# Kernel tuning notes

Hardware: AMD Instinct MI355X
Metric: run time of the kernel (lower is better)

## Reference

```python
import jax, jax.numpy as jnp
import numpy as np

N_NODES = 200000
N_EDGES = 3200000


def _gcn_prep(edge_index, n_nodes):
    # Add self loops (PyG GCNConv default) and compute symmetric normalization.
    loops = jnp.arange(n_nodes, dtype=edge_index.dtype)
    src = jnp.concatenate([edge_index[0], loops])
    dst = jnp.concatenate([edge_index[1], loops])
    deg = jax.ops.segment_sum(jnp.ones_like(dst, dtype=jnp.float32), dst,
                              num_segments=n_nodes)
    dinv = jnp.where(deg > 0, jax.lax.rsqrt(deg), 0.0)
    norm = dinv[src] * dinv[dst]  # [E+N]
    return src, dst, norm


def _gcn_conv(x, src, dst, norm, W, b, n_nodes):
    h = x @ W                                   # [N, out]
    msg = h[src] * norm[:, None]                # gather + scale, [E+N, out]
    out = jax.ops.segment_sum(msg, dst, num_segments=n_nodes)  # scatter-add
    return out + b


def setup_inputs() -> dict:
    key = jax.random.key(0)
    k = jax.random.split(key, 4)
    x = jax.random.normal(k[0], (N_NODES, 4), dtype=jnp.float32)
    edge_index = jax.random.randint(k[1], (2, N_EDGES), 0, N_NODES, dtype=jnp.int64)
    W1 = jax.random.normal(k[2], (4, 16), dtype=jnp.float32) * (1.0 / np.sqrt(4))
    b1 = jnp.zeros((16,), dtype=jnp.float32)
    W2 = jax.random.normal(k[3], (16, 1), dtype=jnp.float32) * (1.0 / np.sqrt(16))
    b2 = jnp.zeros((1,), dtype=jnp.float32)
    return {"x": x, "edge_index": edge_index, "W1": W1, "b1": b1,
            "W2": W2, "b2": b2}


def reference(x, edge_index, W1, b1, W2, b2):
    n = x.shape[0]
    src, dst, norm = _gcn_prep(edge_index, n)
    h = _gcn_conv(x, src, dst, norm, W1, b1, n)
    h = jax.nn.relu(h)
    out = _gcn_conv(h, src, dst, norm, W2, b2, n)
    return out
```

## Files before the change

kernel.cpp:

```cpp
#include <hip/hip_runtime.h>


#define BSE   512
#define CH    16384
#define NBW   512
#define SH    9
#define NB    391
#define FCAP  10752
#define BSB   512
#define RSTG  ((FCAP + BSB - 1) / BSB)
#define NOEDGE 0xFFFFFFFFu

__global__ void k_bin(const int* __restrict__ src, const int* __restrict__ dst,
                      int E, unsigned* __restrict__ gcur,
                      unsigned* __restrict__ epack) {
    __shared__ unsigned cnt[NB];
    __shared__ unsigned cur[NB];
    __shared__ unsigned basec[NB];
    int b = blockIdx.x, t = threadIdx.x;
    for (int i = t; i < NB; i += BSE) cnt[i] = 0;
    __syncthreads();
    int lo = b * CH, hi = min(E, lo + CH);
    int aligned = (hi - lo) & ~3;
    for (int i = lo + 4 * t; i + 3 < hi; i += 4 * BSE) {
        int4 d4 = *(const int4*)(dst + i);
        atomicAdd(&cnt[((unsigned)d4.x) >> SH], 1u);
        atomicAdd(&cnt[((unsigned)d4.y) >> SH], 1u);
        atomicAdd(&cnt[((unsigned)d4.z) >> SH], 1u);
        atomicAdd(&cnt[((unsigned)d4.w) >> SH], 1u);
    }
    for (int i = lo + aligned + t; i < hi; i += BSE)
        atomicAdd(&cnt[((unsigned)dst[i]) >> SH], 1u);
    __syncthreads();
    for (int i = t; i < NB; i += BSE) {
        unsigned c = cnt[i];
        unsigned pad = (c + 15u) & ~15u;
        unsigned ofs = pad ? atomicAdd(&gcur[i], pad) : 0u;
        unsigned base = (unsigned)i * FCAP + ofs;
        basec[i] = base;
        cur[i] = base;
    }
    __syncthreads();
    for (int i = lo + 4 * t; i + 3 < hi; i += 4 * BSE) {
        int4 d4 = *(const int4*)(dst + i);
        int4 s4 = *(const int4*)(src + i);
        unsigned k0 = ((unsigned)d4.x) >> SH, k1 = ((unsigned)d4.y) >> SH;
        unsigned k2 = ((unsigned)d4.z) >> SH, k3 = ((unsigned)d4.w) >> SH;
        unsigned p0 = atomicAdd(&cur[k0], 1u);
        unsigned p1 = atomicAdd(&cur[k1], 1u);
        unsigned p2 = atomicAdd(&cur[k2], 1u);
        unsigned p3 = atomicAdd(&cur[k3], 1u);
        if (p0 < (k0 + 1u) * FCAP) epack[p0] = ((unsigned)s4.x << SH) | (((unsigned)d4.x) & (NBW - 1u));
        if (p1 < (k1 + 1u) * FCAP) epack[p1] = ((unsigned)s4.y << SH) | (((unsigned)d4.y) & (NBW - 1u));
        if (p2 < (k2 + 1u) * FCAP) epack[p2] = ((unsigned)s4.z << SH) | (((unsigned)d4.z) & (NBW - 1u));
        if (p3 < (k3 + 1u) * FCAP) epack[p3] = ((unsigned)s4.w << SH) | (((unsigned)d4.w) & (NBW - 1u));
    }
    for (int i = lo + aligned + t; i < hi; i += BSE) {
        unsigned d = (unsigned)dst[i];
        unsigned k = d >> SH;
        unsigned pos = atomicAdd(&cur[k], 1u);
        if (pos < (k + 1u) * FCAP)
            epack[pos] = ((unsigned)src[i] << SH) | (d & (NBW - 1u));
    }
    __syncthreads();
    for (int i = t; i < NB; i += BSE) {
        unsigned end = basec[i] + ((cnt[i] + 15u) & ~15u);
        unsigned kend = ((unsigned)i + 1u) * FCAP;
        if (end > kend) end = kend;
        for (unsigned p = cur[i]; p < end; ++p) epack[p] = NOEDGE;
    }
}

__global__ void k_build(unsigned* __restrict__ epack, const unsigned* __restrict__ gcur,
                        const float* __restrict__ x,
                        unsigned* __restrict__ rowofs, unsigned* __restrict__ rowcnt,
                        float* __restrict__ x_scaled, int N) {
    __shared__ unsigned stage[FCAP];
    __shared__ unsigned cnt[BSB];
    __shared__ unsigned sc[BSB];
    __shared__ unsigned cur[BSB];
    int k = blockIdx.x, t = threadIdx.x;
    unsigned base = (unsigned)k * FCAP;
    int len = min((int)gcur[k], FCAP);
    for (int i = 4 * t; i + 3 < len; i += 4 * BSB)
        *(int4*)&stage[i] = *(const int4*)(epack + base + i);
    if (t < (len & 3)) stage[(len & ~3) + t] = epack[base + (len & ~3) + t];
    cnt[t] = 0;
    __syncthreads();
    for (int i = t; i < len; i += BSB) {
        unsigned p = stage[i];
        if (p != NOEDGE) atomicAdd(&cnt[p & (NBW - 1u)], 1u);
    }
    __syncthreads();
    unsigned c = cnt[t];
    sc[t] = c;
    __syncthreads();
    for (int off = 1; off < BSB; off <<= 1) {
        unsigned u = (t >= off) ? sc[t - off] : 0;
        __syncthreads();
        sc[t] += u;
        __syncthreads();
    }
    unsigned excl = sc[t] - c;
    cur[t] = excl;
    int node = k * NBW + t;
    if (node < N) {
        rowofs[node] = base + excl;
        rowcnt[node] = c;
        float di = rsqrtf((float)(c + 1));
        float4 xv = ((const float4*)x)[node];
        ((float4*)x_scaled)[node] = make_float4(xv.x * di, xv.y * di, xv.z * di, xv.w * di);
    }
    __syncthreads();
    int lenv = (int)sc[BSB - 1];
    unsigned r[RSTG];
    int nr = 0;
    for (int i = t; i < len; i += BSB) r[nr++] = stage[i];
    __syncthreads();
    for (int j = 0; j < nr; ++j) {
        unsigned p = r[j];
        if (p != NOEDGE) {
            unsigned pos = atomicAdd(&cur[p & (NBW - 1u)], 1u);
            stage[pos] = p >> SH;
        }
    }
    __syncthreads();
    for (int i = 4 * t; i + 3 < lenv; i += 4 * BSB)
        *(int4*)(epack + base + i) = *(const int4*)&stage[i];
    if (t < (lenv & 3)) epack[base + (lenv & ~3) + t] = stage[(lenv & ~3) + t];
}

__global__ void k_agg1(const unsigned* __restrict__ esorted, const unsigned* __restrict__ rowofs,
                       const unsigned* __restrict__ rowcnt,
                       const float* __restrict__ x_scaled,
                       const float* __restrict__ W1, const float* __restrict__ b1,
                       const float* __restrict__ W2,
                       float* __restrict__ z_scaled, int N) {
    int node = blockIdx.x * blockDim.x + threadIdx.x;
    if (node >= N) return;
    unsigned lo = rowofs[node], c = rowcnt[node], hi = lo + c;
    float di = rsqrtf((float)(c + 1));
    const float4* xs4 = (const float4*)x_scaled;
    float4 a0 = xs4[node];
    float4 a1 = make_float4(0.f, 0.f, 0.f, 0.f);
    float4 a2 = make_float4(0.f, 0.f, 0.f, 0.f);
    float4 a3 = make_float4(0.f, 0.f, 0.f, 0.f);
    unsigned i = lo;
    for (; i + 3 < hi; i += 4) {
        float4 v0 = xs4[esorted[i]],     v1 = xs4[esorted[i + 1]];
        float4 v2 = xs4[esorted[i + 2]], v3 = xs4[esorted[i + 3]];
        a0.x += v0.x; a0.y += v0.y; a0.z += v0.z; a0.w += v0.w;
        a1.x += v1.x; a1.y += v1.y; a1.z += v1.z; a1.w += v1.w;
        a2.x += v2.x; a2.y += v2.y; a2.z += v2.z; a2.w += v2.w;
        a3.x += v3.x; a3.y += v3.y; a3.z += v3.z; a3.w += v3.w;
    }
    for (; i < hi; ++i) {
        float4 v = xs4[esorted[i]];
        a0.x += v.x; a0.y += v.y; a0.z += v.z; a0.w += v.w;
    }
    float p0 = di * (a0.x + a1.x + a2.x + a3.x);
    float p1 = di * (a0.y + a1.y + a2.y + a3.y);
    float p2 = di * (a0.z + a1.z + a2.z + a3.z);
    float p3 = di * (a0.w + a1.w + a2.w + a3.w);
    float z = 0.0f;
    #pragma unroll
    for (int cc = 0; cc < 16; ++cc) {
        float h1 = p0 * W1[0 * 16 + cc] + p1 * W1[1 * 16 + cc]
                 + p2 * W1[2 * 16 + cc] + p3 * W1[3 * 16 + cc] + b1[cc];
        h1 = fmaxf(h1, 0.0f);
        z += h1 * W2[cc];
    }
    z_scaled[node] = z * di;
}

__global__ void k_agg2(const unsigned* __restrict__ esorted, const unsigned* __restrict__ rowofs,
                       const unsigned* __restrict__ rowcnt,
                       const float* __restrict__ z_scaled,
                       const float* __restrict__ b2, float* __restrict__ out, int N) {
    int node = blockIdx.x * blockDim.x + threadIdx.x;
    if (node >= N) return;
    unsigned lo = rowofs[node], c = rowcnt[node], hi = lo + c;
    float di = rsqrtf((float)(c + 1));
    float a0 = z_scaled[node], a1 = 0.f, a2 = 0.f, a3 = 0.f;
    unsigned i = lo;
    for (; i + 3 < hi; i += 4) {
        a0 += z_scaled[esorted[i]];
        a1 += z_scaled[esorted[i + 1]];
        a2 += z_scaled[esorted[i + 2]];
        a3 += z_scaled[esorted[i + 3]];
    }
    for (; i < hi; ++i) a0 += z_scaled[esorted[i]];
    out[node] = di * (a0 + a1 + a2 + a3) + b2[0];
}

extern "C" void kernel_launch(void* const* d_in, const int* in_sizes, int n_in,
                              void* d_out, int out_size, void* d_ws, size_t ws_size,
                              hipStream_t stream) {
    const float* x  = (const float*)d_in[0];
    const int*   ei = (const int*)d_in[1];
    const float* W1 = (const float*)d_in[2];
    const float* b1 = (const float*)d_in[3];
    const float* W2 = (const float*)d_in[4];
    const float* b2 = (const float*)d_in[5];

    const int N = in_sizes[0] / 4;
    const int E = in_sizes[1] / 2;
    const int* src = ei;
    const int* dst = ei + E;
    const int NA = (E + CH - 1) / CH;

    char* ws = (char*)d_ws;
    unsigned* gcur      = (unsigned*)ws;  ws += 4096;
    unsigned* epack     = (unsigned*)ws;  ws += (size_t)NB * FCAP * 4;
    unsigned* rowofs    = (unsigned*)ws;  ws += (size_t)N * 4;
    unsigned* rowcnt    = (unsigned*)ws;  ws += (size_t)N * 4;
    float*    x_scaled  = (float*)ws;     ws += (size_t)N * 4 * 4;
    float*    z_scaled  = (float*)ws;     ws += (size_t)N * 4;
    float* out = (float*)d_out;

    hipMemsetAsync(gcur, 0, NB * sizeof(unsigned), stream);
    k_bin  <<<NA, BSE, 0, stream>>>(src, dst, E, gcur, epack);
    k_build<<<NB, BSB, 0, stream>>>(epack, gcur, x, rowofs, rowcnt, x_scaled, N);
    k_agg1 <<<(N + 255) / 256, 256, 0, stream>>>(epack, rowofs, rowcnt, x_scaled,
                                                 W1, b1, W2, z_scaled, N);
    k_agg2 <<<(N + 255) / 256, 256, 0, stream>>>(epack, rowofs, rowcnt, z_scaled,
                                                 b2, out, N);
}
```

Before: 169.9 us.

## Reorder nodes by degree within each bin to balance aggregation warps

Inside k_build, nodes in each 512-node bin are counting-sorted by in-degree (capped at 127) into permuted slots, and their row offset, count and node id are written in that order. The aggregation kernels then iterate over the permuted slots so threads in a wavefront have similar loop trip counts, which cuts divergence. The cost is an extra shared-memory histogram and scan, a node-id indirection, scattered writes of z and out, and an extra zsP array.

```diff
diff --git a/kernel.cpp b/kernel.cpp
--- a/kernel.cpp
+++ b/kernel.cpp
@@ -9,7 +9,9 @@
 #define FCAP  10752
 #define BSB   512
 #define RSTG  ((FCAP + BSB - 1) / BSB)
+#define DMX   128
 #define NOEDGE 0xFFFFFFFFu
+#define INVALID 0xFFFFFFFFu
 
 __global__ void k_bin(const int* __restrict__ src, const int* __restrict__ dst,
                       int E, unsigned* __restrict__ gcur,
@@ -73,12 +75,15 @@
 
 __global__ void k_build(unsigned* __restrict__ epack, const unsigned* __restrict__ gcur,
                         const float* __restrict__ x,
-                        unsigned* __restrict__ rowofs, unsigned* __restrict__ rowcnt,
+                        unsigned* __restrict__ rowofsP, unsigned* __restrict__ rowcntP,
+                        unsigned* __restrict__ nmap,
                         float* __restrict__ x_scaled, int N) {
     __shared__ unsigned stage[FCAP];
     __shared__ unsigned cnt[BSB];
     __shared__ unsigned sc[BSB];
     __shared__ unsigned cur[BSB];
+    __shared__ unsigned dh[DMX];
+    __shared__ unsigned dsc[DMX];
     int k = blockIdx.x, t = threadIdx.x;
     unsigned base = (unsigned)k * FCAP;
     int len = min((int)gcur[k], FCAP);
@@ -86,6 +91,7 @@
         *(int4*)&stage[i] = *(const int4*)(epack + base + i);
     if (t < (len & 3)) stage[(len & ~3) + t] = epack[base + (len & ~3) + t];
     cnt[t] = 0;
+    if (t < DMX) dh[t] = 0;
     __syncthreads();
     for (int i = t; i < len; i += BSB) {
         unsigned p = stage[i];
@@ -105,12 +111,26 @@
     cur[t] = excl;
     int node = k * NBW + t;
     if (node < N) {
-        rowofs[node] = base + excl;
-        rowcnt[node] = c;
         float di = rsqrtf((float)(c + 1));
         float4 xv = ((const float4*)x)[node];
         ((float4*)x_scaled)[node] = make_float4(xv.x * di, xv.y * di, xv.z * di, xv.w * di);
     }
+    unsigned dc = (node < N) ? min(c, (unsigned)(DMX - 1)) : (unsigned)(DMX - 1);
+    unsigned rank = atomicAdd(&dh[dc], 1u);
+    __syncthreads();
+    if (t < DMX) dsc[t] = dh[t];
+    __syncthreads();
+    for (int off = 1; off < DMX; off <<= 1) {
+        unsigned u = (t < DMX && t >= off) ? dsc[t - off] : 0;
+        __syncthreads();
+        if (t < DMX) dsc[t] += u;
+        __syncthreads();
+    }
+    unsigned slot = (dc ? dsc[dc - 1] : 0u) + rank;
+    unsigned gslot = (unsigned)k * NBW + slot;
+    rowofsP[gslot] = base + excl;
+    rowcntP[gslot] = c;
+    nmap[gslot] = (node < N) ? (unsigned)node : INVALID;
     __syncthreads();
     int lenv = (int)sc[BSB - 1];
     unsigned r[RSTG];
@@ -130,15 +150,17 @@
     if (t < (lenv & 3)) epack[base + (lenv & ~3) + t] = stage[(lenv & ~3) + t];
 }
 
-__global__ void k_agg1(const unsigned* __restrict__ esorted, const unsigned* __restrict__ rowofs,
-                       const unsigned* __restrict__ rowcnt,
+__global__ void k_agg1(const unsigned* __restrict__ esorted, const unsigned* __restrict__ rowofsP,
+                       const unsigned* __restrict__ rowcntP, const unsigned* __restrict__ nmap,
                        const float* __restrict__ x_scaled,
                        const float* __restrict__ W1, const float* __restrict__ b1,
                        const float* __restrict__ W2,
-                       float* __restrict__ z_scaled, int N) {
-    int node = blockIdx.x * blockDim.x + threadIdx.x;
-    if (node >= N) return;
-    unsigned lo = rowofs[node], c = rowcnt[node], hi = lo + c;
+                       float* __restrict__ z_scaled, float* __restrict__ zsP, int NS) {
+    int gs = blockIdx.x * blockDim.x + threadIdx.x;
+    if (gs >= NS) return;
+    unsigned node = nmap[gs];
+    if (node == INVALID) return;
+    unsigned lo = rowofsP[gs], c = rowcntP[gs], hi = lo + c;
     float di = rsqrtf((float)(c + 1));
     const float4* xs4 = (const float4*)x_scaled;
     float4 a0 = xs4[node];
@@ -170,18 +192,22 @@
         h1 = fmaxf(h1, 0.0f);
         z += h1 * W2[cc];
     }
-    z_scaled[node] = z * di;
-}
-
-__global__ void k_agg2(const unsigned* __restrict__ esorted, const unsigned* __restrict__ rowofs,
-                       const unsigned* __restrict__ rowcnt,
-                       const float* __restrict__ z_scaled,
-                       const float* __restrict__ b2, float* __restrict__ out, int N) {
-    int node = blockIdx.x * blockDim.x + threadIdx.x;
-    if (node >= N) return;
-    unsigned lo = rowofs[node], c = rowcnt[node], hi = lo + c;
+    float zs = z * di;
+    z_scaled[node] = zs;
+    zsP[gs] = zs;
+}
+
+__global__ void k_agg2(const unsigned* __restrict__ esorted, const unsigned* __restrict__ rowofsP,
+                       const unsigned* __restrict__ rowcntP, const unsigned* __restrict__ nmap,
+                       const float* __restrict__ z_scaled, const float* __restrict__ zsP,
+                       const float* __restrict__ b2, float* __restrict__ out, int NS) {
+    int gs = blockIdx.x * blockDim.x + threadIdx.x;
+    if (gs >= NS) return;
+    unsigned node = nmap[gs];
+    if (node == INVALID) return;
+    unsigned lo = rowofsP[gs], c = rowcntP[gs], hi = lo + c;
     float di = rsqrtf((float)(c + 1));
-    float a0 = z_scaled[node], a1 = 0.f, a2 = 0.f, a3 = 0.f;
+    float a0 = zsP[gs], a1 = 0.f, a2 = 0.f, a3 = 0.f;
     unsigned i = lo;
     for (; i + 3 < hi; i += 4) {
         a0 += z_scaled[esorted[i]];
@@ -208,21 +234,24 @@
     const int* src = ei;
     const int* dst = ei + E;
     const int NA = (E + CH - 1) / CH;
+    const int NS = NB * NBW;
 
     char* ws = (char*)d_ws;
     unsigned* gcur      = (unsigned*)ws;  ws += 4096;
     unsigned* epack     = (unsigned*)ws;  ws += (size_t)NB * FCAP * 4;
-    unsigned* rowofs    = (unsigned*)ws;  ws += (size_t)N * 4;
-    unsigned* rowcnt    = (unsigned*)ws;  ws += (size_t)N * 4;
+    unsigned* rowofsP   = (unsigned*)ws;  ws += (size_t)NS * 4;
+    unsigned* rowcntP   = (unsigned*)ws;  ws += (size_t)NS * 4;
+    unsigned* nmap      = (unsigned*)ws;  ws += (size_t)NS * 4;
+    float*    zsP       = (float*)ws;     ws += (size_t)NS * 4;
     float*    x_scaled  = (float*)ws;     ws += (size_t)N * 4 * 4;
     float*    z_scaled  = (float*)ws;     ws += (size_t)N * 4;
     float* out = (float*)d_out;
 
     hipMemsetAsync(gcur, 0, NB * sizeof(unsigned), stream);
     k_bin  <<<NA, BSE, 0, stream>>>(src, dst, E, gcur, epack);
-    k_build<<<NB, BSB, 0, stream>>>(epack, gcur, x, rowofs, rowcnt, x_scaled, N);
-    k_agg1 <<<(N + 255) / 256, 256, 0, stream>>>(epack, rowofs, rowcnt, x_scaled,
-                                                 W1, b1, W2, z_scaled, N);
-    k_agg2 <<<(N + 255) / 256, 256, 0, stream>>>(epack, rowofs, rowcnt, z_scaled,
-                                                 b2, out, N);
-}
+    k_build<<<NB, BSB, 0, stream>>>(epack, gcur, x, rowofsP, rowcntP, nmap, x_scaled, N);
+    k_agg1 <<<(NS + 255) / 256, 256, 0, stream>>>(epack, rowofsP, rowcntP, nmap, x_scaled,
+                                                  W1, b1, W2, z_scaled, zsP, NS);
+    k_agg2 <<<(NS + 255) / 256, 256, 0, stream>>>(epack, rowofsP, rowcntP, nmap, z_scaled,
+                                                  zsP, b2, out, NS);
+}
```

After: 192.8 us. 13.5% more time.
